# Kernel tuning notes

Measured on AMD Instinct MI355X. Metric: run time of the kernel, lower is better.

Reference implementation:

```python
import jax, jax.numpy as jnp
from jax import lax
import numpy as np

B, CIN, COUT, H, W = 16, 128, 256, 64, 64
E, K, RED = 4, 3, 4

def setup_inputs() -> dict:
    key = jax.random.key(0)
    ks = jax.random.split(key, 16)
    s = 0.05
    return {
        'x': jax.random.normal(ks[0], (B, CIN, H, W), jnp.float32),
        'expert_w': jax.random.normal(ks[1], (E, COUT, CIN, K, K), jnp.float32) * s,
        'r1_w': jax.random.normal(ks[2], (E // 2, CIN), jnp.float32) * s,
        'r1_b': jnp.zeros((E // 2,), jnp.float32),
        'r2_w': jax.random.normal(ks[3], (E, E // 2), jnp.float32) * s,
        'r2_b': jnp.zeros((E,), jnp.float32),
        'r3_w': jax.random.normal(ks[4], (E, E), jnp.float32) * s,
        'r3_b': jnp.zeros((E,), jnp.float32),
        'ca1_w': jax.random.normal(ks[5], (COUT // RED, COUT), jnp.float32) * s,
        'ca1_b': jnp.zeros((COUT // RED,), jnp.float32),
        'ca2_w': jax.random.normal(ks[6], (COUT, COUT // RED), jnp.float32) * s,
        'ca2_b': jnp.zeros((COUT,), jnp.float32),
        'sa_w': jax.random.normal(ks[7], (1, COUT, 7, 7), jnp.float32) * s,
        'sa_b': jnp.zeros((1,), jnp.float32),
        'bn_gamma': jnp.ones((COUT,), jnp.float32),
        'bn_beta': jnp.zeros((COUT,), jnp.float32),
    }

def _conv(x, w, stride, pad):
    return lax.conv_general_dilated(x, w, (stride, stride), [(pad, pad), (pad, pad)],
                                     dimension_numbers=('NCHW', 'OIHW', 'NCHW'))

def reference(x, expert_w, r1_w, r1_b, r2_w, r2_b, r3_w, r3_b,
              ca1_w, ca1_b, ca2_w, ca2_b, sa_w, sa_b, bn_gamma, bn_beta):
    # --- routing: GAP -> 1x1 convs (as matmuls) -> softmax over experts ---
    g = x.mean(axis=(2, 3))                                   # [B, Cin]
    h = jax.nn.relu(g @ r1_w.T + r1_b)
    h = jax.nn.relu(h @ r2_w.T + r2_b)
    rw = jax.nn.softmax(h @ r3_w.T + r3_b, axis=1)            # [B, E]
    # --- all experts as one stacked conv, then weighted combine ---
    w = expert_w.reshape(E * COUT, CIN, K, K)
    y = _conv(x, w, 1, 1)                                     # [B, E*Cout, H, W]
    y = y.reshape(x.shape[0], E, COUT, y.shape[2], y.shape[3])
    out = jnp.einsum('be,bechw->bchw', rw, y)                 # [B, Cout, H, W]
    # --- channel attention (SE) ---
    p = out.mean(axis=(2, 3))                                  # [B, Cout]
    ca = jax.nn.sigmoid(jax.nn.relu(p @ ca1_w.T + ca1_b) @ ca2_w.T + ca2_b)
    # --- spatial attention: 7x7 conv -> sigmoid ---
    sa = jax.nn.sigmoid(_conv(out, sa_w, 1, 3) + sa_b[None, :, None, None])  # [B,1,H,W]
    out = out * ca[:, :, None, None] * sa
    # --- BatchNorm (training mode: batch statistics) + ReLU ---
    mean = out.mean(axis=(0, 2, 3))
    var = out.var(axis=(0, 2, 3))
    out = (out - mean[None, :, None, None]) * lax.rsqrt(var + 1e-5)[None, :, None, None]
    out = out * bn_gamma[None, :, None, None] + bn_beta[None, :, None, None]
    return jax.nn.relu(out)
```

## Files before the change

### kernel.cpp

```cpp
#include <hip/hip_runtime.h>
#include <math.h>

#define B_    16
#define CIN_  128
#define COUT_ 256
#define H_    64
#define W_    64
#define HW_   4096

typedef __attribute__((ext_vector_type(8))) short short8v;
typedef __attribute__((ext_vector_type(4))) float f32x4;

#define WS_GPX     0
#define WS_RW      131072
#define WS_CP      131136
#define WS_CA      196672
#define WS_PSUM    200768
#define WS_PSQ     204864
#define WS_BNSCALE 208960
#define WS_BNSHIFT 209216
#define WS_SA      209472
#define WS_WSA     275008
#define WS_WCB_F   283200
#define WS_XT_F    2642496
#define WS_U_F     WS_XT_F

static __device__ __forceinline__ unsigned short f2bf(float f) {
    union { float f; unsigned int u; } v; v.f = f;
    unsigned int u = v.u;
    return (unsigned short)((u + 0x7FFFu + ((u >> 16) & 1u)) >> 16);
}

__device__ __forceinline__ void gl16(const void* g, const void* l) {
    __builtin_amdgcn_global_load_lds(
        (const __attribute__((address_space(1))) unsigned int*)g,
        (__attribute__((address_space(3))) unsigned int*)l, 16, 0, 0);
}

__global__ __launch_bounds__(256) void k_xt(const float* __restrict__ x,
                                            unsigned short* __restrict__ xt,
                                            float* __restrict__ gpart) {
    int h = blockIdx.x, b = blockIdx.y;
    int t = threadIdx.x;
    int w = t & 63, c8 = t >> 6;
    unsigned short* xtb = xt + (size_t)b * 66*66*128;
    unsigned short* orow = xtb + (((size_t)(h+1))*66 + (w+1))*128;
    float* gp = gpart + ((size_t)b*64 + h)*128;
    #pragma unroll
    for (int i = 0; i < 4; ++i) {
        int ci0 = i*32 + c8*8;
        float f[8];
        short8v vv;
        #pragma unroll
        for (int j = 0; j < 8; ++j) {
            f[j] = x[(((size_t)b*CIN_ + ci0 + j)*H_ + h)*W_ + w];
            vv[j] = (short)f2bf(f[j]);
        }
        *(short8v*)(orow + ci0) = vv;
        #pragma unroll
        for (int j = 0; j < 8; ++j) {
            float s = f[j];
            s += __shfl_down(s, 32, 64);
            s += __shfl_down(s, 16, 64);
            s += __shfl_down(s, 8, 64);
            s += __shfl_down(s, 4, 64);
            s += __shfl_down(s, 2, 64);
            s += __shfl_down(s, 1, 64);
            f[j] = s;
        }
        if (w == 0) {
            #pragma unroll
            for (int j = 0; j < 8; ++j) gp[ci0 + j] = f[j];
        }
    }
    xtb[(((size_t)(h+1))*66 + (t >> 7)*65)*128 + (t & 127)] = 0;
    if (h == 0 || h == 63) {
        int r = (h == 0) ? 0 : 65;
        unsigned short* rowp = xtb + ((size_t)r*66)*128;
        for (int i = t; i < 1056; i += 256)
            *(short8v*)(rowp + (size_t)i*8) = (short8v){0,0,0,0,0,0,0,0};
    }
}

__global__ void k_route(const float* __restrict__ gpart,
                        const float* r1w, const float* r1b,
                        const float* r2w, const float* r2b,
                        const float* r3w, const float* r3b,
                        float* __restrict__ rw) {
    int b = blockIdx.x;
    int t = threadIdx.x;
    __shared__ float gl_[128];
    float s = 0.f;
    for (int h = 0; h < 64; ++h) s += gpart[((size_t)b*64 + h)*128 + t];
    gl_[t] = s * (1.f/4096.f);
    __syncthreads();
    if (t == 0) {
        float h1[2];
        for (int j = 0; j < 2; ++j) {
            float acc = r1b[j];
            for (int c = 0; c < CIN_; ++c) acc += gl_[c]*r1w[j*CIN_+c];
            h1[j] = fmaxf(acc, 0.f);
        }
        float h2[4];
        for (int e = 0; e < 4; ++e)
            h2[e] = fmaxf(r2b[e] + h1[0]*r2w[e*2] + h1[1]*r2w[e*2+1], 0.f);
        float lg[4], m = -1e30f;
        for (int e = 0; e < 4; ++e) {
            float acc = r3b[e];
            for (int j = 0; j < 4; ++j) acc += h2[j]*r3w[e*4+j];
            lg[e] = acc; m = fmaxf(m, acc);
        }
        float den = 0.f;
        for (int e = 0; e < 4; ++e) { lg[e] = expf(lg[e]-m); den += lg[e]; }
        float inv = 1.f/den;
        for (int e = 0; e < 4; ++e) rw[b*4+e] = lg[e]*inv;
    }
}

__global__ __launch_bounds__(256) void k_wcomb(const float* __restrict__ ew,
                                               const float* __restrict__ rw,
                                               unsigned short* __restrict__ wc,
                                               const float* __restrict__ saw,
                                               unsigned short* __restrict__ wsa) {
    int t = threadIdx.x;
    if (blockIdx.x >= COUT_) {
        int i = (blockIdx.x - COUT_)*256 + t;
        int tap = i >> 8, c = i & 255;
        float v = (tap < 49) ? saw[c*49 + tap] : 0.f;
        wsa[tap*256 + c] = f2bf(v);
        return;
    }
    int co = blockIdx.x;
    __shared__ float ewl[4*1152];
    __shared__ float rwl[64];
    #pragma unroll
    for (int e = 0; e < 4; ++e) {
        const float* src = ew + ((size_t)(e*COUT_ + co))*1152;
        for (int i = t; i < 1152; i += 256) ewl[e*1152 + i] = src[i];
    }
    if (t < 64) rwl[t] = rw[t];
    __syncthreads();
    for (int i = 0; i < 72; ++i) {
        int f = i*256 + t;
        int b = f / 1152;
        int rem = f - b*1152;
        int tap = rem >> 7, ci = rem & 127;
        int lidx = ci*9 + tap;
        float v = rwl[b*4+0]*ewl[0*1152+lidx] + rwl[b*4+1]*ewl[1*1152+lidx]
                + rwl[b*4+2]*ewl[2*1152+lidx] + rwl[b*4+3]*ewl[3*1152+lidx];
        wc[((size_t)(b*9 + tap)*COUT_ + co)*128 + ci] = f2bf(v);
    }
}

__global__ __launch_bounds__(256) void k_conv(const unsigned short* __restrict__ xt,
                                              const unsigned short* __restrict__ wc,
                                              float* __restrict__ out,
                                              float* __restrict__ cpart) {
    __shared__ unsigned short xs[1600*8];
    __shared__ unsigned short wl[2304*8];
    __shared__ float gsl[4][64];
    int ht = blockIdx.x;
    int cb = blockIdx.y;
    int b  = blockIdx.z;
    int t  = threadIdx.x;
    int wv = t >> 6, lane = t & 63;
    int lr = lane & 15, kq = lane >> 4;
    int h0 = ht * 4;

    const unsigned short* xtb = xt + (size_t)b * 66*66*128;
    const unsigned short* wcb = wc + (size_t)b * 9*256*128;

    int wboff = (lr >> 1)*128 + ((((lr & 1) << 2) + kq) ^ (lr >> 1))*16;

    f32x4 acc[4][4];
    #pragma unroll
    for (int m = 0; m < 4; ++m)
        #pragma unroll
        for (int n = 0; n < 4; ++n) acc[m][n] = (f32x4){0.f,0.f,0.f,0.f};

    for (int ci0 = 0; ci0 < CIN_; ci0 += 32) {
        __syncthreads();
        for (int j = wv; j < 25; j += 4) {
            int s = j*64 + lane;
            if (s > 1583) s = 1583;
            int P = s >> 3, cph = s & 7;
            int clg = cph ^ (P & 7);
            int pos = P*2 + (clg >> 2), kq2 = clg & 3;
            int rp = pos / 66, cp = pos - rp*66;
            const unsigned short* g = xtb + (((size_t)(h0+rp)*66 + cp)*128 + ci0 + kq2*8);
            gl16(g, (const char*)xs + (size_t)j*1024);
        }
        for (int j = wv; j < 36; j += 4) {
            int s = j*64 + lane;
            int P = s >> 3, cph = s & 7;
            int clg = cph ^ (P & 7);
            int R = P*2 + (clg >> 2);
            int tap = R >> 6, col = R & 63, kq2 = clg & 3;
            const unsigned short* g = wcb + (((size_t)tap*COUT_ + cb*64 + col)*128 + ci0 + kq2*8);
            gl16(g, (const char*)wl + (size_t)j*1024);
        }
        asm volatile("s_waitcnt vmcnt(0)" ::: "memory");
        __syncthreads();

        #pragma unroll
        for (int dh = 0; dh < 3; ++dh) {
            #pragma unroll
            for (int dw = 0; dw < 3; ++dw) {
                int tap = dh*3 + dw;
                int pos0 = (wv + dh)*66 + lr + dw;
                int p2 = pos0 >> 1;
                int xboff = p2*128 + ((((pos0 & 1) << 2) + kq) ^ (p2 & 7))*16;
                short8v af[4], bfv[4];
                #pragma unroll
                for (int m = 0; m < 4; ++m)
                    af[m] = *(const short8v*)((const char*)wl + tap*4096 + m*1024 + wboff);
                #pragma unroll
                for (int n = 0; n < 4; ++n)
                    bfv[n] = *(const short8v*)((const char*)xs + xboff + n*1024);
                #pragma unroll
                for (int m = 0; m < 4; ++m)
                    #pragma unroll
                    for (int n = 0; n < 4; ++n)
                        acc[m][n] = __builtin_amdgcn_mfma_f32_16x16x32_bf16(
                            af[m], bfv[n], acc[m][n], 0, 0, 0);
            }
        }
    }

    float* ob = out + ((size_t)b*COUT_ + cb*64)*HW_ + (h0 + wv)*W_;
    #pragma unroll
    for (int m = 0; m < 4; ++m)
        #pragma unroll
        for (int n = 0; n < 4; ++n) {
            f32x4 v = acc[m][n];
            #pragma unroll
            for (int r = 0; r < 4; ++r)
                ob[(size_t)(m*16 + kq*4 + r)*HW_ + n*16 + lr] = v[r];
        }

    float gp[4][4];
    #pragma unroll
    for (int m = 0; m < 4; ++m)
        #pragma unroll
        for (int r = 0; r < 4; ++r)
            gp[m][r] = acc[m][0][r] + acc[m][1][r] + acc[m][2][r] + acc[m][3][r];
    #pragma unroll
    for (int o = 8; o > 0; o >>= 1)
        #pragma unroll
        for (int m = 0; m < 4; ++m)
            #pragma unroll
            for (int r = 0; r < 4; ++r)
                gp[m][r] += __shfl_down(gp[m][r], o, 64);
    if ((lane & 15) == 0) {
        #pragma unroll
        for (int m = 0; m < 4; ++m)
            #pragma unroll
            for (int r = 0; r < 4; ++r)
                gsl[wv][m*16 + kq*4 + r] = gp[m][r];
    }
    __syncthreads();
    if (t < 64) {
        float s = gsl[0][t] + gsl[1][t] + gsl[2][t] + gsl[3][t];
        cpart[((size_t)b*16 + ht)*COUT_ + cb*64 + t] = s;
    }
}

__global__ void k_ca(const float* __restrict__ cpart, const float* ca1w, const float* ca1b,
                     const float* ca2w, const float* ca2b, float* __restrict__ ca) {
    int b = blockIdx.x;
    int t = threadIdx.x;
    __shared__ float pfull[256];
    __shared__ float h1[64];
    for (int i = t; i < 256; i += 64) {
        float s = 0.f;
        for (int h = 0; h < 16; ++h) s += cpart[((size_t)b*16 + h)*COUT_ + i];
        pfull[i] = s * (1.f/(float)HW_);
    }
    __syncthreads();
    float s = ca1b[t];
    for (int c = 0; c < COUT_; ++c) s += pfull[c] * ca1w[t*COUT_ + c];
    h1[t] = fmaxf(s, 0.f);
    __syncthreads();
    for (int i = 0; i < 4; ++i) {
        int co = t*4 + i;
        float s2 = ca2b[co];
        for (int j = 0; j < 64; ++j) s2 += h1[j] * ca2w[co*64 + j];
        ca[b*COUT_ + co] = 1.f/(1.f + expf(-s2));
    }
}

__global__ __launch_bounds__(256) void k_sa_gemm(const float* __restrict__ mix,
                                                 const unsigned short* __restrict__ wsa,
                                                 float* __restrict__ u) {
    __shared__ unsigned short wl[16384];
    __shared__ unsigned short bt[16384];
    int pxt = blockIdx.x;
    int b   = blockIdx.y;
    int t = threadIdx.x, wv = t >> 6, lane = t & 63;
    int lr = lane & 15, kq = lane >> 4;
    int px0 = pxt * 64;

    #pragma unroll
    for (int k = 0; k < 8; ++k) {
        int s = t + k*256;
        int row = s >> 5, cs = s & 31;
        short8v v = *(const short8v*)(wsa + row*256 + cs*8);
        int off = row*512 + ((cs*16) ^ ((row & 7) << 4));
        *(short8v*)((char*)wl + off) = v;
    }
    {
        int px = lane;
        const float* mb = mix + ((size_t)b*COUT_)*HW_ + px0 + px;
        #pragma unroll
        for (int c8 = 0; c8 < 8; ++c8) {
            int cb = wv*64 + c8*8;
            short8v v;
            #pragma unroll
            for (int j = 0; j < 8; ++j)
                v[j] = (short)f2bf(mb[(size_t)(cb + j)*HW_]);
            int off = px*512 + ((cb*2) ^ ((px & 7) << 4));
            *(short8v*)((char*)bt + off) = v;
        }
    }
    __syncthreads();

    f32x4 acc[4];
    #pragma unroll
    for (int n = 0; n < 4; ++n) acc[n] = (f32x4){0.f,0.f,0.f,0.f};

    #pragma unroll
    for (int ks = 0; ks < 8; ++ks) {
        int ci0 = ks*32;
        int arow = wv*16 + lr;
        short8v a = *(const short8v*)((const char*)wl +
                        arow*512 + (((ci0 + kq*8)*2) ^ ((arow & 7) << 4)));
        #pragma unroll
        for (int n = 0; n < 4; ++n) {
            int prow = n*16 + lr;
            short8v bv = *(const short8v*)((const char*)bt +
                            prow*512 + (((ci0 + kq*8)*2) ^ ((prow & 7) << 4)));
            acc[n] = __builtin_amdgcn_mfma_f32_16x16x32_bf16(a, bv, acc[n], 0, 0, 0);
        }
    }

    float* ub = u + (size_t)b*64*HW_;
    #pragma unroll
    for (int n = 0; n < 4; ++n)
        #pragma unroll
        for (int r = 0; r < 4; ++r)
            ub[(size_t)(wv*16 + kq*4 + r)*HW_ + px0 + n*16 + lr] = acc[n][r];
}

__global__ void k_sared(const float* __restrict__ u, const float* __restrict__ sab,
                        float* __restrict__ sa) {
    int b = blockIdx.y;
    int h = blockIdx.x * 4 + (threadIdx.x >> 6);
    int w = threadIdx.x & 63;
    float s = sab[0];
    const float* ub = u + (size_t)b*64*HW_;
    #pragma unroll
    for (int dh = 0; dh < 7; ++dh) {
        int hh = h + dh - 3;
        if (hh < 0 || hh >= H_) continue;
        #pragma unroll
        for (int dw = 0; dw < 7; ++dw) {
            int ww = w + dw - 3;
            if (ww < 0 || ww >= W_) continue;
            s += ub[(size_t)(dh*7 + dw)*HW_ + hh*W_ + ww];
        }
    }
    sa[(size_t)b*HW_ + h*W_ + w] = 1.f/(1.f + expf(-s));
}

__global__ void k_stats(const float* __restrict__ io, const float* __restrict__ ca,
                        const float* __restrict__ sa,
                        float* __restrict__ psum, float* __restrict__ psq) {
    int c = blockIdx.x & 255;
    int b = blockIdx.x >> 8;
    float cav = ca[b*COUT_ + c];
    const float* pl = io + ((size_t)b*COUT_ + c) * HW_;
    const float* sab = sa + (size_t)b * HW_;
    float s = 0.f, sq = 0.f;
    for (int i = threadIdx.x; i < HW_/4; i += 256) {
        float4 v = ((const float4*)pl)[i];
        float4 w = ((const float4*)sab)[i];
        v.x *= cav*w.x; v.y *= cav*w.y; v.z *= cav*w.z; v.w *= cav*w.w;
        s  += v.x+v.y+v.z+v.w;
        sq += v.x*v.x+v.y*v.y+v.z*v.z+v.w*v.w;
    }
    for (int o = 32; o > 0; o >>= 1) { s += __shfl_down(s,o,64); sq += __shfl_down(sq,o,64); }
    __shared__ float ls[8];
    int wid = threadIdx.x>>6, lane = threadIdx.x&63;
    if (lane==0) { ls[wid]=s; ls[4+wid]=sq; }
    __syncthreads();
    if (threadIdx.x==0) {
        psum[b*COUT_+c] = ls[0]+ls[1]+ls[2]+ls[3];
        psq [b*COUT_+c] = ls[4]+ls[5]+ls[6]+ls[7];
    }
}

__global__ void k_bnfin(const float* __restrict__ psum, const float* __restrict__ psq,
                        const float* __restrict__ gamma, const float* __restrict__ beta,
                        float* __restrict__ scale, float* __restrict__ shift) {
    int c = threadIdx.x;
    float s=0.f, q=0.f;
    for (int b = 0; b < B_; ++b) { s += psum[b*COUT_+c]; q += psq[b*COUT_+c]; }
    float n = (float)(B_*HW_);
    float mean = s/n;
    float var = q/n - mean*mean;
    float sc = gamma[c] * rsqrtf(var + 1e-5f);
    scale[c] = sc;
    shift[c] = beta[c] - mean*sc;
}

__global__ void k_bnapply(float* __restrict__ io, const float* __restrict__ ca,
                          const float* __restrict__ sa,
                          const float* __restrict__ scale, const float* __restrict__ shift) {
    size_t i = (size_t)blockIdx.x * 256 + threadIdx.x;
    int c = (int)((i >> 10) & 255);
    int b = (int)(i >> 18);
    int px4 = (int)(i & 1023);
    float cav = ca[b*COUT_ + c];
    float sc = scale[c], sh = shift[c];
    float4 v = ((float4*)io)[i];
    float4 w = ((const float4*)(sa + (size_t)b*HW_))[px4];
    v.x = fmaxf(fmaf(v.x*cav*w.x, sc, sh), 0.f);
    v.y = fmaxf(fmaf(v.y*cav*w.y, sc, sh), 0.f);
    v.z = fmaxf(fmaf(v.z*cav*w.z, sc, sh), 0.f);
    v.w = fmaxf(fmaf(v.w*cav*w.w, sc, sh), 0.f);
    ((float4*)io)[i] = v;
}

extern "C" void kernel_launch(void* const* d_in, const int* in_sizes, int n_in,
                              void* d_out, int out_size, void* d_ws, size_t ws_size,
                              hipStream_t stream) {
    const float* x    = (const float*)d_in[0];
    const float* ew   = (const float*)d_in[1];
    const float* r1w  = (const float*)d_in[2];
    const float* r1b  = (const float*)d_in[3];
    const float* r2w  = (const float*)d_in[4];
    const float* r2b  = (const float*)d_in[5];
    const float* r3w  = (const float*)d_in[6];
    const float* r3b  = (const float*)d_in[7];
    const float* ca1w = (const float*)d_in[8];
    const float* ca1b = (const float*)d_in[9];
    const float* ca2w = (const float*)d_in[10];
    const float* ca2b = (const float*)d_in[11];
    const float* saw  = (const float*)d_in[12];
    const float* sab  = (const float*)d_in[13];
    const float* gm   = (const float*)d_in[14];
    const float* bt   = (const float*)d_in[15];
    float* out = (float*)d_out;
    float* ws  = (float*)d_ws;
    unsigned short* wcb = (unsigned short*)(ws + WS_WCB_F);
    unsigned short* xt  = (unsigned short*)(ws + WS_XT_F);
    unsigned short* wsa = (unsigned short*)(ws + WS_WSA);
    float* u = ws + WS_U_F;

    k_xt<<<dim3(64,16), 256, 0, stream>>>(x, xt, ws+WS_GPX);
    k_route<<<16, 128, 0, stream>>>(ws+WS_GPX, r1w, r1b, r2w, r2b, r3w, r3b, ws+WS_RW);
    k_wcomb<<<320, 256, 0, stream>>>(ew, ws+WS_RW, wcb, saw, wsa);
    k_conv<<<dim3(16,4,16), 256, 0, stream>>>(xt, wcb, out, ws+WS_CP);
    k_ca<<<B_, 64, 0, stream>>>(ws+WS_CP, ca1w, ca1b, ca2w, ca2b, ws+WS_CA);
    k_sa_gemm<<<dim3(64,16), 256, 0, stream>>>(out, wsa, u);
    k_sared<<<dim3(16,16), 256, 0, stream>>>(u, sab, ws+WS_SA);
    k_stats<<<B_*COUT_, 256, 0, stream>>>(out, ws+WS_CA, ws+WS_SA, ws+WS_PSUM, ws+WS_PSQ);
    k_bnfin<<<1, 256, 0, stream>>>(ws+WS_PSUM, ws+WS_PSQ, gm, bt, ws+WS_BNSCALE, ws+WS_BNSHIFT);
    k_bnapply<<<16384, 256, 0, stream>>>(out, ws+WS_CA, ws+WS_SA, ws+WS_BNSCALE, ws+WS_BNSHIFT);
}
```

Baseline: 165.9 us.

## Store conv mix output as bf16 intermediate and drop LDS swizzle

The conv kernel now writes its combined expert output as bf16 to a workspace buffer instead of fp32 into the output tensor. The spatial-attention GEMM, stats, and BN-apply kernels read that bf16 buffer, halving intermediate traffic and removing a conversion in the SA GEMM. The XOR swizzle on LDS tiles in the conv kernel is also removed in favour of a linear layout, which may introduce LDS bank conflicts. BN statistics and the final output are now computed from rounded bf16 values, which lowers precision.

```diff
diff --git a/kernel.cpp b/kernel.cpp
--- a/kernel.cpp
+++ b/kernel.cpp
@@ -24,11 +24,16 @@
 #define WS_WCB_F   283200
 #define WS_XT_F    2642496
 #define WS_U_F     WS_XT_F
+#define WS_MIX_F   7103040
 
 static __device__ __forceinline__ unsigned short f2bf(float f) {
     union { float f; unsigned int u; } v; v.f = f;
     unsigned int u = v.u;
     return (unsigned short)((u + 0x7FFFu + ((u >> 16) & 1u)) >> 16);
+}
+static __device__ __forceinline__ float bf2f(unsigned short h) {
+    union { unsigned int u; float f; } v; v.u = ((unsigned int)h) << 16;
+    return v.f;
 }
 
 __device__ __forceinline__ void gl16(const void* g, const void* l) {
@@ -154,7 +159,7 @@
 
 __global__ __launch_bounds__(256) void k_conv(const unsigned short* __restrict__ xt,
                                               const unsigned short* __restrict__ wc,
-                                              float* __restrict__ out,
+                                              unsigned short* __restrict__ mixb,
                                               float* __restrict__ cpart) {
     __shared__ unsigned short xs[1600*8];
     __shared__ unsigned short wl[2304*8];
@@ -170,8 +175,6 @@
     const unsigned short* xtb = xt + (size_t)b * 66*66*128;
     const unsigned short* wcb = wc + (size_t)b * 9*256*128;
 
-    int wboff = (lr >> 1)*128 + ((((lr & 1) << 2) + kq) ^ (lr >> 1))*16;
-
     f32x4 acc[4][4];
     #pragma unroll
     for (int m = 0; m < 4; ++m)
@@ -183,20 +186,15 @@
         for (int j = wv; j < 25; j += 4) {
             int s = j*64 + lane;
             if (s > 1583) s = 1583;
-            int P = s >> 3, cph = s & 7;
-            int clg = cph ^ (P & 7);
-            int pos = P*2 + (clg >> 2), kq2 = clg & 3;
+            int pos = s >> 2, q = s & 3;
             int rp = pos / 66, cp = pos - rp*66;
-            const unsigned short* g = xtb + (((size_t)(h0+rp)*66 + cp)*128 + ci0 + kq2*8);
+            const unsigned short* g = xtb + (((size_t)(h0 + rp)*66 + cp)*128 + ci0 + q*8);
             gl16(g, (const char*)xs + (size_t)j*1024);
         }
         for (int j = wv; j < 36; j += 4) {
             int s = j*64 + lane;
-            int P = s >> 3, cph = s & 7;
-            int clg = cph ^ (P & 7);
-            int R = P*2 + (clg >> 2);
-            int tap = R >> 6, col = R & 63, kq2 = clg & 3;
-            const unsigned short* g = wcb + (((size_t)tap*COUT_ + cb*64 + col)*128 + ci0 + kq2*8);
+            int tap = s >> 8, col = (s >> 2) & 63, q = s & 3;
+            const unsigned short* g = wcb + (((size_t)tap*COUT_ + cb*64 + col)*128 + ci0 + q*8);
             gl16(g, (const char*)wl + (size_t)j*1024);
         }
         asm volatile("s_waitcnt vmcnt(0)" ::: "memory");
@@ -207,16 +205,13 @@
             #pragma unroll
             for (int dw = 0; dw < 3; ++dw) {
                 int tap = dh*3 + dw;
-                int pos0 = (wv + dh)*66 + lr + dw;
-                int p2 = pos0 >> 1;
-                int xboff = p2*128 + ((((pos0 & 1) << 2) + kq) ^ (p2 & 7))*16;
                 short8v af[4], bfv[4];
                 #pragma unroll
                 for (int m = 0; m < 4; ++m)
-                    af[m] = *(const short8v*)((const char*)wl + tap*4096 + m*1024 + wboff);
+                    af[m] = *(const short8v*)(wl + ((size_t)tap*2048 + (m*16 + lr)*32 + kq*8));
                 #pragma unroll
                 for (int n = 0; n < 4; ++n)
-                    bfv[n] = *(const short8v*)((const char*)xs + xboff + n*1024);
+                    bfv[n] = *(const short8v*)(xs + ((size_t)(wv+dh)*2112 + (n*16 + lr + dw)*32 + kq*8));
                 #pragma unroll
                 for (int m = 0; m < 4; ++m)
                     #pragma unroll
@@ -227,7 +222,7 @@
         }
     }
 
-    float* ob = out + ((size_t)b*COUT_ + cb*64)*HW_ + (h0 + wv)*W_;
+    unsigned short* ob = mixb + ((size_t)b*COUT_ + cb*64)*HW_ + (h0 + wv)*W_;
     #pragma unroll
     for (int m = 0; m < 4; ++m)
         #pragma unroll
@@ -235,7 +230,7 @@
             f32x4 v = acc[m][n];
             #pragma unroll
             for (int r = 0; r < 4; ++r)
-                ob[(size_t)(m*16 + kq*4 + r)*HW_ + n*16 + lr] = v[r];
+                ob[(size_t)(m*16 + kq*4 + r)*HW_ + n*16 + lr] = f2bf(v[r]);
         }
 
     float gp[4][4];
@@ -289,7 +284,7 @@
     }
 }
 
-__global__ __launch_bounds__(256) void k_sa_gemm(const float* __restrict__ mix,
+__global__ __launch_bounds__(256) void k_sa_gemm(const unsigned short* __restrict__ mixb,
                                                  const unsigned short* __restrict__ wsa,
                                                  float* __restrict__ u) {
     __shared__ unsigned short wl[16384];
@@ -310,14 +305,14 @@
     }
     {
         int px = lane;
-        const float* mb = mix + ((size_t)b*COUT_)*HW_ + px0 + px;
+        const unsigned short* mb = mixb + (size_t)b*COUT_*HW_ + px0 + px;
         #pragma unroll
         for (int c8 = 0; c8 < 8; ++c8) {
             int cb = wv*64 + c8*8;
             short8v v;
             #pragma unroll
             for (int j = 0; j < 8; ++j)
-                v[j] = (short)f2bf(mb[(size_t)(cb + j)*HW_]);
+                v[j] = (short)mb[(size_t)(cb + j)*HW_];
             int off = px*512 + ((cb*2) ^ ((px & 7) << 4));
             *(short8v*)((char*)bt + off) = v;
         }
@@ -372,21 +367,29 @@
     sa[(size_t)b*HW_ + h*W_ + w] = 1.f/(1.f + expf(-s));
 }
 
-__global__ void k_stats(const float* __restrict__ io, const float* __restrict__ ca,
+__global__ void k_stats(const unsigned short* __restrict__ mixb, const float* __restrict__ ca,
                         const float* __restrict__ sa,
                         float* __restrict__ psum, float* __restrict__ psq) {
     int c = blockIdx.x & 255;
     int b = blockIdx.x >> 8;
     float cav = ca[b*COUT_ + c];
-    const float* pl = io + ((size_t)b*COUT_ + c) * HW_;
+    const unsigned short* pl = mixb + ((size_t)b*COUT_ + c) * HW_;
     const float* sab = sa + (size_t)b * HW_;
     float s = 0.f, sq = 0.f;
-    for (int i = threadIdx.x; i < HW_/4; i += 256) {
-        float4 v = ((const float4*)pl)[i];
-        float4 w = ((const float4*)sab)[i];
-        v.x *= cav*w.x; v.y *= cav*w.y; v.z *= cav*w.z; v.w *= cav*w.w;
-        s  += v.x+v.y+v.z+v.w;
-        sq += v.x*v.x+v.y*v.y+v.z*v.z+v.w*v.w;
+    for (int i = threadIdx.x; i < HW_/8; i += 256) {
+        short8v v = ((const short8v*)pl)[i];
+        float4 w0 = ((const float4*)sab)[2*i];
+        float4 w1 = ((const float4*)sab)[2*i+1];
+        float f0 = bf2f((unsigned short)v[0])*cav*w0.x;
+        float f1 = bf2f((unsigned short)v[1])*cav*w0.y;
+        float f2 = bf2f((unsigned short)v[2])*cav*w0.z;
+        float f3 = bf2f((unsigned short)v[3])*cav*w0.w;
+        float f4 = bf2f((unsigned short)v[4])*cav*w1.x;
+        float f5 = bf2f((unsigned short)v[5])*cav*w1.y;
+        float f6 = bf2f((unsigned short)v[6])*cav*w1.z;
+        float f7 = bf2f((unsigned short)v[7])*cav*w1.w;
+        s  += f0+f1+f2+f3+f4+f5+f6+f7;
+        sq += f0*f0+f1*f1+f2*f2+f3*f3+f4*f4+f5*f5+f6*f6+f7*f7;
     }
     for (int o = 32; o > 0; o >>= 1) { s += __shfl_down(s,o,64); sq += __shfl_down(sq,o,64); }
     __shared__ float ls[8];
@@ -413,22 +416,29 @@
     shift[c] = beta[c] - mean*sc;
 }
 
-__global__ void k_bnapply(float* __restrict__ io, const float* __restrict__ ca,
-                          const float* __restrict__ sa,
+__global__ void k_bnapply(const unsigned short* __restrict__ mixb, float* __restrict__ out,
+                          const float* __restrict__ ca, const float* __restrict__ sa,
                           const float* __restrict__ scale, const float* __restrict__ shift) {
     size_t i = (size_t)blockIdx.x * 256 + threadIdx.x;
-    int c = (int)((i >> 10) & 255);
-    int b = (int)(i >> 18);
-    int px4 = (int)(i & 1023);
+    int c = (int)((i >> 9) & 255);
+    int b = (int)(i >> 17);
+    int px8 = (int)(i & 511);
     float cav = ca[b*COUT_ + c];
     float sc = scale[c], sh = shift[c];
-    float4 v = ((float4*)io)[i];
-    float4 w = ((const float4*)(sa + (size_t)b*HW_))[px4];
-    v.x = fmaxf(fmaf(v.x*cav*w.x, sc, sh), 0.f);
-    v.y = fmaxf(fmaf(v.y*cav*w.y, sc, sh), 0.f);
-    v.z = fmaxf(fmaf(v.z*cav*w.z, sc, sh), 0.f);
-    v.w = fmaxf(fmaf(v.w*cav*w.w, sc, sh), 0.f);
-    ((float4*)io)[i] = v;
+    short8v v = ((const short8v*)mixb)[i];
+    const float4* sp = (const float4*)(sa + (size_t)b*HW_) + (size_t)px8*2;
+    float4 w0 = sp[0], w1 = sp[1];
+    float4 o0, o1;
+    o0.x = fmaxf(fmaf(bf2f((unsigned short)v[0])*cav*w0.x, sc, sh), 0.f);
+    o0.y = fmaxf(fmaf(bf2f((unsigned short)v[1])*cav*w0.y, sc, sh), 0.f);
+    o0.z = fmaxf(fmaf(bf2f((unsigned short)v[2])*cav*w0.z, sc, sh), 0.f);
+    o0.w = fmaxf(fmaf(bf2f((unsigned short)v[3])*cav*w0.w, sc, sh), 0.f);
+    o1.x = fmaxf(fmaf(bf2f((unsigned short)v[4])*cav*w1.x, sc, sh), 0.f);
+    o1.y = fmaxf(fmaf(bf2f((unsigned short)v[5])*cav*w1.y, sc, sh), 0.f);
+    o1.z = fmaxf(fmaf(bf2f((unsigned short)v[6])*cav*w1.z, sc, sh), 0.f);
+    o1.w = fmaxf(fmaf(bf2f((unsigned short)v[7])*cav*w1.w, sc, sh), 0.f);
+    ((float4*)out)[i*2]   = o0;
+    ((float4*)out)[i*2+1] = o1;
 }
 
 extern "C" void kernel_launch(void* const* d_in, const int* in_sizes, int n_in,
@@ -452,19 +462,20 @@
     const float* bt   = (const float*)d_in[15];
     float* out = (float*)d_out;
     float* ws  = (float*)d_ws;
-    unsigned short* wcb = (unsigned short*)(ws + WS_WCB_F);
-    unsigned short* xt  = (unsigned short*)(ws + WS_XT_F);
-    unsigned short* wsa = (unsigned short*)(ws + WS_WSA);
+    unsigned short* wcb  = (unsigned short*)(ws + WS_WCB_F);
+    unsigned short* xt   = (unsigned short*)(ws + WS_XT_F);
+    unsigned short* wsa  = (unsigned short*)(ws + WS_WSA);
+    unsigned short* mixb = (unsigned short*)(ws + WS_MIX_F);
     float* u = ws + WS_U_F;
 
     k_xt<<<dim3(64,16), 256, 0, stream>>>(x, xt, ws+WS_GPX);
     k_route<<<16, 128, 0, stream>>>(ws+WS_GPX, r1w, r1b, r2w, r2b, r3w, r3b, ws+WS_RW);
     k_wcomb<<<320, 256, 0, stream>>>(ew, ws+WS_RW, wcb, saw, wsa);
-    k_conv<<<dim3(16,4,16), 256, 0, stream>>>(xt, wcb, out, ws+WS_CP);
+    k_conv<<<dim3(16,4,16), 256, 0, stream>>>(xt, wcb, mixb, ws+WS_CP);
     k_ca<<<B_, 64, 0, stream>>>(ws+WS_CP, ca1w, ca1b, ca2w, ca2b, ws+WS_CA);
-    k_sa_gemm<<<dim3(64,16), 256, 0, stream>>>(out, wsa, u);
+    k_sa_gemm<<<dim3(64,16), 256, 0, stream>>>(mixb, wsa, u);
     k_sared<<<dim3(16,16), 256, 0, stream>>>(u, sab, ws+WS_SA);
-    k_stats<<<B_*COUT_, 256, 0, stream>>>(out, ws+WS_CA, ws+WS_SA, ws+WS_PSUM, ws+WS_PSQ);
+    k_stats<<<B_*COUT_, 256, 0, stream>>>(mixb, ws+WS_CA, ws+WS_SA, ws+WS_PSUM, ws+WS_PSQ);
     k_bnfin<<<1, 256, 0, stream>>>(ws+WS_PSUM, ws+WS_PSQ, gm, bt, ws+WS_BNSCALE, ws+WS_BNSHIFT);
-    k_bnapply<<<16384, 256, 0, stream>>>(out, ws+WS_CA, ws+WS_SA, ws+WS_BNSCALE, ws+WS_BNSHIFT);
-}
+    k_bnapply<<<8192, 256, 0, stream>>>(mixb, out, ws+WS_CA, ws+WS_SA, ws+WS_BNSCALE, ws+WS_BNSHIFT);
+}
```

After: 152.3 us. -8.2%, faster.
